# Optimization experiments

Hardware: AMD Instinct MI355X
Metric: run time of the kernel (lower is better)

Reference implementation:

```python
import jax, jax.numpy as jnp
import numpy as np

N, E = 50000, 300000
IN, FC, AC, H, C1, C2, OUT = 1024, 128, 20, 4, 10, 5, 3
FCN = FC + AC + H * C2  # 168


def bn_eval(x, g, b):
    # BatchNorm1d in eval mode with running_mean=0, running_var=1
    return x * (g / jnp.sqrt(1.0 + 1e-5)) + b


def add_self_loops(edge_index, edge_attr, n):
    # PyG add_self_loops with fill_value='mean': self-loop attr = mean of incoming edge attrs
    src, dst = edge_index[0], edge_index[1]
    ones = jnp.ones(src.shape[0], jnp.float32)
    deg = jax.ops.segment_sum(ones, dst, num_segments=n)
    mean_attr = jax.ops.segment_sum(edge_attr, dst, num_segments=n) / jnp.maximum(deg, 1.0)[:, None]
    loop = jnp.arange(n, dtype=src.dtype)
    return (jnp.concatenate([src, loop]), jnp.concatenate([dst, loop]),
            jnp.concatenate([edge_attr, mean_attr], 0))


def gatv2(x, src, dst, eattr, Wl, bl, Wr, br, We, att, b, n):
    # GATv2Conv (concat=True, negative_slope=0.2, edge_dim=1)
    h, c = att.shape
    xl = (x @ Wl + bl).reshape(n, h, c)
    xr = (x @ Wr + br).reshape(n, h, c)
    em = (eattr @ We).reshape(-1, h, c)
    m = jax.nn.leaky_relu(xl[src] + xr[dst] + em, 0.2)   # [E', H, C]
    logit = jnp.einsum('ehc,hc->eh', m, att)              # [E', H]
    mx = jax.ops.segment_max(logit, dst, num_segments=n)
    ex = jnp.exp(logit - mx[dst])
    den = jax.ops.segment_sum(ex, dst, num_segments=n)
    alpha = ex / (den[dst] + 1e-16)                       # segment softmax over dst
    out = jax.ops.segment_sum(xl[src] * alpha[..., None], dst, num_segments=n)
    return out.reshape(n, h * c) + b


def setup_inputs() -> dict:
    key = jax.random.key(0)
    ks = jax.random.split(key, 24)
    rn = lambda k, s: jax.random.normal(k, s, jnp.float32) * 0.05
    return {
        'features': jax.random.normal(ks[0], (N, IN), jnp.float32),
        'edges': jax.random.randint(ks[1], (2, E), 0, N),
        'edges2': jax.random.randint(ks[2], (2, E), 0, N),
        'edge_features': jax.random.normal(ks[3], (E, 1), jnp.float32),
        'additional_features': jax.random.normal(ks[4], (N, AC), jnp.float32),
        'sage_Wl': rn(ks[5], (IN, FC)), 'sage_bl': jnp.zeros((FC,), jnp.float32),
        'sage_Wr': rn(ks[6], (IN, FC)),
        'g1_Wl': rn(ks[7], (AC, H * C1)), 'g1_bl': jnp.zeros((H * C1,), jnp.float32),
        'g1_Wr': rn(ks[8], (AC, H * C1)), 'g1_br': jnp.zeros((H * C1,), jnp.float32),
        'g1_We': rn(ks[9], (1, H * C1)), 'g1_att': rn(ks[10], (H, C1)),
        'g1_b': jnp.zeros((H * C1,), jnp.float32),
        'g2_Wl': rn(ks[11], (H * C1, H * C2)), 'g2_bl': jnp.zeros((H * C2,), jnp.float32),
        'g2_Wr': rn(ks[12], (H * C1, H * C2)), 'g2_br': jnp.zeros((H * C2,), jnp.float32),
        'g2_We': rn(ks[13], (1, H * C2)), 'g2_att': rn(ks[14], (H, C2)),
        'g2_b': jnp.zeros((H * C2,), jnp.float32),
        'fc1_W': rn(ks[15], (FCN, FCN)), 'fc1_b': jnp.zeros((FCN,), jnp.float32),
        'fc2_W': rn(ks[16], (FCN, OUT)), 'fc2_b': jnp.zeros((OUT,), jnp.float32),
        'bnx_g': jnp.ones((FC,), jnp.float32), 'bnx_b': jnp.zeros((FC,), jnp.float32),
        'bny_g': jnp.ones((H * C2,), jnp.float32), 'bny_b': jnp.zeros((H * C2,), jnp.float32),
        'bnf_g': jnp.ones((FCN,), jnp.float32), 'bnf_b': jnp.zeros((FCN,), jnp.float32),
    }


def reference(features, edges, edges2, edge_features, additional_features,
              sage_Wl, sage_bl, sage_Wr,
              g1_Wl, g1_bl, g1_Wr, g1_br, g1_We, g1_att, g1_b,
              g2_Wl, g2_bl, g2_Wr, g2_br, g2_We, g2_att, g2_b,
              fc1_W, fc1_b, fc2_W, fc2_b,
              bnx_g, bnx_b, bny_g, bny_b, bnf_g, bnf_b):
    n = features.shape[0]
    # --- SAGEConv (mean aggr): out = lin_l(mean_j x_j) + lin_r(x_i) ---
    src, dst = edges[0], edges[1]
    deg = jax.ops.segment_sum(jnp.ones(src.shape[0], jnp.float32), dst, num_segments=n)
    aggr = jax.ops.segment_sum(features[src], dst, num_segments=n) / jnp.maximum(deg, 1.0)[:, None]
    x = aggr @ sage_Wl + sage_bl + features @ sage_Wr
    x = bn_eval(x, bnx_g, bnx_b)
    # --- GATv2 stack (self loops with mean edge-attr fill) ---
    s2, d2, ea = add_self_loops(edges2, edge_features, n)
    y = gatv2(additional_features, s2, d2, ea, g1_Wl, g1_bl, g1_Wr, g1_br, g1_We, g1_att, g1_b, n)
    y = jax.nn.leaky_relu(y, 0.01)  # activation (dropout off in eval)
    y = gatv2(y, s2, d2, ea, g2_Wl, g2_bl, g2_Wr, g2_br, g2_We, g2_att, g2_b, n)
    y = bn_eval(y, bny_g, bny_b)
    # --- MLP head ---
    z = jax.nn.leaky_relu(jnp.concatenate([x, y], axis=1), 0.01)
    z = jnp.concatenate([z, additional_features], axis=1) @ fc1_W + fc1_b
    z = jax.nn.relu(bn_eval(z, bnf_g, bnf_b))
    return z @ fc2_W + fc2_b
```

## Files before the change

### kernel.cpp

```cpp
#include <hip/hip_runtime.h>
#include <hip/hip_bf16.h>
#include <cfloat>

__device__ __forceinline__ float lrelu(float x, float a) { return x > 0.0f ? x : a * x; }

__device__ __forceinline__ unsigned short f2bf(float f) {
    unsigned u = __float_as_uint(f);
    unsigned r = (u + 0x7FFFu + ((u >> 16) & 1u)) >> 16;
    return (unsigned short)r;
}
__device__ __forceinline__ float bf2f(unsigned short u) {
    return __uint_as_float((unsigned)u << 16);
}

typedef __attribute__((ext_vector_type(8))) short short8;
typedef __attribute__((ext_vector_type(4))) float f32x4;

#define BN_RSQ 0.99999500003749968750f
#define SCAN_B 256

__global__ void zero_ws(uint4* __restrict__ p, int n16)
{
    int t = blockIdx.x * blockDim.x + threadIdx.x;
    if (t < n16) p[t] = make_uint4(0u, 0u, 0u, 0u);
}

__global__ void conv_wsage(const float* __restrict__ Wl, const float* __restrict__ Wr,
                           unsigned short* __restrict__ Btp)
{
    int idx = blockIdx.x * blockDim.x + threadIdx.x;
    if (idx >= 256 * 1024) return;
    int j    = idx & 7;
    int lane = (idx >> 3) & 63;
    int fn   = (idx >> 9) & 3;
    int wid  = (idx >> 11) & 3;
    int t    = idx >> 13;
    int c = wid * 64 + fn * 16 + (lane & 15);
    int k = t * 32 + (lane >> 4) * 8 + j;
    float v = (c < 128) ? Wl[(size_t)k * 128 + c] : Wr[(size_t)k * 128 + (c - 128)];
    Btp[idx] = f2bf(v);
}

__global__ void conv_wfc1(const float* __restrict__ fc1W, unsigned short* __restrict__ Bt1p)
{
    int idx = blockIdx.x * blockDim.x + threadIdx.x;
    if (idx >= 36864) return;
    int j    = idx & 7;
    int lane = (idx >> 3) & 63;
    int fn   = (idx >> 9) & 3;
    int q    = idx >> 11;
    int wid = q % 3, t = q / 3;
    int c = wid * 64 + fn * 16 + (lane & 15);
    int k = t * 32 + (lane >> 4) * 8 + j;
    float v = (c < 168 && k < 168) ? fc1W[(size_t)k * 168 + c] : 0.0f;
    Bt1p[idx] = f2bf(v);
}

__global__ __launch_bounds__(256) void gemm_sage_mfma(
    const float* __restrict__ A, const unsigned short* __restrict__ Btp,
    unsigned short* __restrict__ P, int M)
{
    __shared__ unsigned short As2[2][64][72];
    const int tid = threadIdx.x;
    const int wid = tid >> 6, lane = tid & 63;
    const int m0 = blockIdx.x * 64;
    const int l16 = lane & 15, g = lane >> 4;
    const int colbase = wid * 64 + l16;
    const short8* Bv = reinterpret_cast<const short8*>(Btp);
    const int srow = tid >> 4, scol = (tid & 15) * 4;

    f32x4 acc[4][4] = {};
    float4 rcur[4], rnext[4];

#pragma unroll
    for (int p = 0; p < 4; ++p) {
        int ar = m0 + p * 16 + srow;
        rcur[p] = make_float4(0.f, 0.f, 0.f, 0.f);
        if (ar < M) rcur[p] = *reinterpret_cast<const float4*>(&A[(size_t)ar * 1024 + scol]);
    }
#pragma unroll
    for (int p = 0; p < 4; ++p) {
        ushort4 u;
        u.x = f2bf(rcur[p].x); u.y = f2bf(rcur[p].y); u.z = f2bf(rcur[p].z); u.w = f2bf(rcur[p].w);
        *reinterpret_cast<ushort4*>(&As2[0][p * 16 + srow][scol]) = u;
    }
#pragma unroll
    for (int p = 0; p < 4; ++p) {
        int ar = m0 + p * 16 + srow;
        rcur[p] = make_float4(0.f, 0.f, 0.f, 0.f);
        if (ar < M) rcur[p] = *reinterpret_cast<const float4*>(&A[(size_t)ar * 1024 + 64 + scol]);
    }
    __syncthreads();

    for (int c = 0; c < 16; ++c) {
        const int buf = c & 1;
        short8 bfr[2][4];
#pragma unroll
        for (int t = 0; t < 2; ++t)
#pragma unroll
            for (int fn = 0; fn < 4; ++fn)
                bfr[t][fn] = Bv[(((c * 2 + t) * 4 + wid) * 4 + fn) * 64 + lane];
        __builtin_amdgcn_sched_barrier(0);
        if (c < 14) {
            const int k0 = (c + 2) * 64;
#pragma unroll
            for (int p = 0; p < 4; ++p) {
                int ar = m0 + p * 16 + srow;
                rnext[p] = make_float4(0.f, 0.f, 0.f, 0.f);
                if (ar < M) rnext[p] = *reinterpret_cast<const float4*>(&A[(size_t)ar * 1024 + k0 + scol]);
            }
        }
        __builtin_amdgcn_sched_barrier(0);
#pragma unroll
        for (int t = 0; t < 2; ++t) {
            short8 afr[4];
#pragma unroll
            for (int fm = 0; fm < 4; ++fm)
                afr[fm] = *reinterpret_cast<const short8*>(&As2[buf][fm * 16 + l16][t * 32 + g * 8]);
#pragma unroll
            for (int fm = 0; fm < 4; ++fm)
#pragma unroll
                for (int fn = 0; fn < 4; ++fn)
                    acc[fm][fn] = __builtin_amdgcn_mfma_f32_16x16x32_bf16(
                        afr[fm], bfr[t][fn], acc[fm][fn], 0, 0, 0);
        }
        if (c < 15) {
#pragma unroll
            for (int p = 0; p < 4; ++p) {
                ushort4 u;
                u.x = f2bf(rcur[p].x); u.y = f2bf(rcur[p].y);
                u.z = f2bf(rcur[p].z); u.w = f2bf(rcur[p].w);
                *reinterpret_cast<ushort4*>(&As2[buf ^ 1][p * 16 + srow][scol]) = u;
            }
        }
        __syncthreads();
#pragma unroll
        for (int p = 0; p < 4; ++p) rcur[p] = rnext[p];
    }

#pragma unroll
    for (int fm = 0; fm < 4; ++fm) {
#pragma unroll
        for (int r = 0; r < 4; ++r) {
            int row = m0 + fm * 16 + g * 4 + r;
            if (row < M) {
#pragma unroll
                for (int fn = 0; fn < 4; ++fn)
                    P[(size_t)row * 256 + colbase + fn * 16] = f2bf(acc[fm][fn][r]);
            }
        }
    }
}

__global__ __launch_bounds__(256) void mlp_mfma(
    const unsigned short* __restrict__ z, const float* __restrict__ addf,
    const unsigned short* __restrict__ Bt1p,
    const float* __restrict__ fc1b, const float* __restrict__ bnfg, const float* __restrict__ bnfb,
    const float* __restrict__ fc2W, const float* __restrict__ fc2b,
    float* __restrict__ out, int M)
{
    __shared__ __align__(16) char smem[64 * 169 * 4];
    unsigned short (*zs)[200] = reinterpret_cast<unsigned short(*)[200]>(smem);
    float (*ts)[169] = reinterpret_cast<float(*)[169]>(smem);
    const int tid = threadIdx.x;
    const int wid = tid >> 6, lane = tid & 63;
    const int m0 = blockIdx.x * 64;
    const int l16 = lane & 15, g = lane >> 4;
    const short8* Bv = reinterpret_cast<const short8*>(Bt1p);

#pragma unroll
    for (int p = 0; p < 13; ++p) {
        int idx = p * 256 + tid;
        if (idx < 3200) {
            int row = idx / 50, c4 = (idx % 50) * 4;
            int ar = m0 + row;
            ushort4 u; u.x = 0; u.y = 0; u.z = 0; u.w = 0;
            if (ar < M) {
                if (c4 < 148) {
                    u = *reinterpret_cast<const ushort4*>(&z[(size_t)ar * 168 + c4]);
                } else if (c4 < 168) {
                    float4 v = *reinterpret_cast<const float4*>(&addf[(size_t)ar * 20 + (c4 - 148)]);
                    u.x = f2bf(v.x); u.y = f2bf(v.y); u.z = f2bf(v.z); u.w = f2bf(v.w);
                }
            }
            *reinterpret_cast<ushort4*>(&zs[row][c4]) = u;
        }
    }
    __syncthreads();

    f32x4 acc[4][4] = {};
    if (wid < 3) {
#pragma unroll
        for (int t = 0; t < 6; ++t) {
            short8 afr[4], bfr[4];
#pragma unroll
            for (int fm = 0; fm < 4; ++fm)
                afr[fm] = *reinterpret_cast<const short8*>(&zs[fm * 16 + l16][t * 32 + g * 8]);
#pragma unroll
            for (int fn = 0; fn < 4; ++fn)
                bfr[fn] = Bv[((t * 3 + wid) * 4 + fn) * 64 + lane];
#pragma unroll
            for (int fm = 0; fm < 4; ++fm)
#pragma unroll
                for (int fn = 0; fn < 4; ++fn)
                    acc[fm][fn] = __builtin_amdgcn_mfma_f32_16x16x32_bf16(
                        afr[fm], bfr[fn], acc[fm][fn], 0, 0, 0);
        }
    }
    __syncthreads();
    if (wid < 3) {
        const int colbase = wid * 64 + l16;
#pragma unroll
        for (int fm = 0; fm < 4; ++fm) {
#pragma unroll
            for (int r = 0; r < 4; ++r) {
                int rr = fm * 16 + g * 4 + r;
#pragma unroll
                for (int fn = 0; fn < 4; ++fn) {
                    int col = colbase + fn * 16;
                    if (col < 168) {
                        float v = acc[fm][fn][r] + fc1b[col];
                        v = v * (bnfg[col] * BN_RSQ) + bnfb[col];
                        ts[rr][col] = fmaxf(v, 0.0f);
                    }
                }
            }
        }
    }
    __syncthreads();
    if (tid < 192) {
        int r = tid & 63, c = tid >> 6;
        float acc2 = fc2b[c];
#pragma unroll 4
        for (int k = 0; k < 168; ++k) acc2 += ts[r][k] * fc2W[k * 3 + c];
        int row = m0 + r;
        if (row < M) out[(size_t)row * 3 + c] = acc2;
    }
}

__global__ void edge_count(const int* __restrict__ e1d, const int* __restrict__ e2d,
                           const float* __restrict__ ef,
                           int* __restrict__ cnt1, int* __restrict__ cnt2,
                           float* __restrict__ easum, float* __restrict__ eaext, int E)
{
    int e = blockIdx.x * blockDim.x + threadIdx.x;
    if (e >= E) return;
    atomicAdd(&cnt1[e1d[e]], 1);
    int d2 = e2d[e];
    atomicAdd(&cnt2[d2], 1);
    float a = ef[e];
    atomicAdd(&easum[d2], a);
    eaext[e] = a;
}

__global__ void scan1(const int* __restrict__ cnt1, const int* __restrict__ cnt2,
                      int* __restrict__ off1, int* __restrict__ off2,
                      int* __restrict__ bsum1, int* __restrict__ bsum2, int M)
{
    __shared__ int sh[SCAN_B];
    int y = blockIdx.y;
    const int* cnt = y ? cnt2 : cnt1;
    int* excl = y ? off2 : off1;
    int* bsum = y ? bsum2 : bsum1;
    int i = blockIdx.x * SCAN_B + threadIdx.x;
    int v = (i < M) ? cnt[i] + y : 0;
    sh[threadIdx.x] = v;
    __syncthreads();
    for (int o = 1; o < SCAN_B; o <<= 1) {
        int t = (threadIdx.x >= o) ? sh[threadIdx.x - o] : 0;
        __syncthreads();
        sh[threadIdx.x] += t;
        __syncthreads();
    }
    if (i < M) excl[i] = sh[threadIdx.x] - v;
    if (threadIdx.x == SCAN_B - 1) bsum[blockIdx.x] = sh[threadIdx.x];
}

__global__ void scan2(int* __restrict__ bsum1, int* __restrict__ bsum2, int nb)
{
    __shared__ int sh[SCAN_B];
    int* bsum = blockIdx.y ? bsum2 : bsum1;
    int v = ((int)threadIdx.x < nb) ? bsum[threadIdx.x] : 0;
    sh[threadIdx.x] = v;
    __syncthreads();
    for (int o = 1; o < SCAN_B; o <<= 1) {
        int t = (threadIdx.x >= o) ? sh[threadIdx.x - o] : 0;
        __syncthreads();
        sh[threadIdx.x] += t;
        __syncthreads();
    }
    if ((int)threadIdx.x < nb) bsum[threadIdx.x] = sh[threadIdx.x] - v;
}

__global__ void scan3(int* __restrict__ off1, int* __restrict__ off2,
                      const int* __restrict__ bsum1, const int* __restrict__ bsum2,
                      const int* __restrict__ cnt1, const int* __restrict__ cnt2,
                      const float* __restrict__ easum, float* __restrict__ eaext,
                      int E, int M)
{
    int y = blockIdx.y;
    int* off = y ? off2 : off1;
    const int* bsum = y ? bsum2 : bsum1;
    const int* cnt = y ? cnt2 : cnt1;
    int i = blockIdx.x * SCAN_B + threadIdx.x;
    if (i < M) {
        int v = off[i] + bsum[blockIdx.x];
        off[i] = v;
        if (i == M - 1) off[M] = v + cnt[i] + y;
        if (y) eaext[E + i] = easum[i] / fmaxf((float)cnt2[i], 1.0f);
    }
}

__global__ void fill_both(const int* __restrict__ e1s, const int* __restrict__ e1d,
                          const int* __restrict__ e2d,
                          const int* __restrict__ off1, const int* __restrict__ off2,
                          int* __restrict__ cnt1, int* __restrict__ cnt2,
                          int* __restrict__ srcs1, int* __restrict__ eidx2, int E, int Eext)
{
    int t = blockIdx.x * blockDim.x + threadIdx.x;
    if (t < E) {
        int d = e1d[t];
        int pos = atomicSub(&cnt1[d], 1) - 1;
        srcs1[off1[d] + pos] = e1s[t];
    }
    int t2 = t - E;
    if (t2 >= 0 && t2 < Eext) {
        if (t2 < E) {
            int d = e2d[t2];
            int pos = atomicSub(&cnt2[d], 1) - 1;
            eidx2[off2[d] + pos] = t2;
        } else {
            int nn = t2 - E;
            eidx2[off2[nn + 1] - 1] = t2;
        }
    }
}

__global__ void sage_gather(const int* __restrict__ srcs1, const int* __restrict__ off1,
                            const unsigned short* __restrict__ P, const float* __restrict__ bl,
                            const float* __restrict__ bng, const float* __restrict__ bnb,
                            unsigned short* __restrict__ z, int N)
{
    int t = blockIdx.x * blockDim.x + threadIdx.x;
    if (t >= N * 32) return;
    int n = t >> 5, g = t & 31;
    int beg = off1[n], end = off1[n + 1];
    float a0 = 0.f, a1 = 0.f, a2 = 0.f, a3 = 0.f;
    for (int j = beg; j < end; ++j) {
        int s = srcs1[j];
        ushort4 v = *reinterpret_cast<const ushort4*>(&P[(size_t)s * 256 + g * 4]);
        a0 += bf2f(v.x); a1 += bf2f(v.y); a2 += bf2f(v.z); a3 += bf2f(v.w);
    }
    float inv = 1.0f / fmaxf((float)(end - beg), 1.0f);
    ushort4 pr = *reinterpret_cast<const ushort4*>(&P[(size_t)n * 256 + 128 + g * 4]);
    float a4[4] = {a0, a1, a2, a3};
    float p4[4] = {bf2f(pr.x), bf2f(pr.y), bf2f(pr.z), bf2f(pr.w)};
    ushort4 zo;
    unsigned short* zp = reinterpret_cast<unsigned short*>(&zo);
#pragma unroll
    for (int k = 0; k < 4; ++k) {
        int cc = g * 4 + k;
        float x = a4[k] * inv + bl[cc] + p4[k];
        x = x * (bng[cc] * BN_RSQ) + bnb[cc];
        zp[k] = f2bf(lrelu(x, 0.01f));
    }
    *reinterpret_cast<ushort4*>(&z[(size_t)n * 168 + g * 4]) = zo;
}

template <int IND, int HC>
__global__ void gat_lin(const float* __restrict__ X,
                        const float* __restrict__ Wl, const float* __restrict__ bl,
                        const float* __restrict__ Wr, const float* __restrict__ br,
                        float* __restrict__ xl, float* __restrict__ xr, int N)
{
    int t = blockIdx.x * blockDim.x + threadIdx.x;
    if (t >= N * HC) return;
    int n = t / HC, j = t % HC;
    float al = bl[j], ar = br[j];
    const float* xrow = X + (size_t)n * IND;
#pragma unroll 4
    for (int k = 0; k < IND; ++k) {
        float xv = xrow[k];
        al += xv * Wl[k * HC + j];
        ar += xv * Wr[k * HC + j];
    }
    xl[t] = al;
    xr[t] = ar;
}

template <int H, int C, int MODE>
__global__ void gat_node(const int* __restrict__ eidx2, const int* __restrict__ off2,
                         const int* __restrict__ e2s, const float* __restrict__ eaext,
                         const float* __restrict__ xl, const float* __restrict__ xr,
                         const float* __restrict__ We, const float* __restrict__ att,
                         const float* __restrict__ b,
                         const float* __restrict__ bng, const float* __restrict__ bnb,
                         void* __restrict__ outv, int E, int N)
{
    int t = blockIdx.x * blockDim.x + threadIdx.x;
    if (t >= N * H) return;
    int n = t / H, h = t % H;

    float xrc[C], atth[C], weh[C];
#pragma unroll
    for (int c = 0; c < C; ++c) {
        xrc[c]  = xr[(size_t)n * (H * C) + h * C + c];
        atth[c] = att[h * C + c];
        weh[c]  = We[h * C + c];
    }

    const int beg = off2[n], end = off2[n + 1];

    float mx = -FLT_MAX, den = 0.0f;
    float accv[C] = {};
    for (int j = beg; j < end; ++j) {
        int e = eidx2[j];
        int s = (e < E) ? e2s[e] : (e - E);
        float ea = eaext[e];
        const float* xls = xl + (size_t)s * (H * C) + h * C;
        float xv[C];
        float lg = 0.0f;
#pragma unroll
        for (int c = 0; c < C; ++c) {
            xv[c] = xls[c];
            float m = xv[c] + xrc[c] + ea * weh[c];
            lg += lrelu(m, 0.2f) * atth[c];
        }
        if (lg > mx) {
            float sc = __expf(mx - lg);
            den *= sc;
#pragma unroll
            for (int c = 0; c < C; ++c) accv[c] *= sc;
            mx = lg;
        }
        float ex = __expf(lg - mx);
        den += ex;
#pragma unroll
        for (int c = 0; c < C; ++c) accv[c] += ex * xv[c];
    }
    float inv = 1.0f / (den + 1e-16f);

#pragma unroll
    for (int c = 0; c < C; ++c) {
        int jch = h * C + c;
        float v = accv[c] * inv + b[jch];
        if (MODE == 1) {
            ((float*)outv)[(size_t)n * (H * C) + jch] = lrelu(v, 0.01f);
        } else {
            v = v * (bng[jch] * BN_RSQ) + bnb[jch];
            ((unsigned short*)outv)[(size_t)n * 168 + 128 + jch] = f2bf(lrelu(v, 0.01f));
        }
    }
}

extern "C" void kernel_launch(void* const* d_in, const int* in_sizes, int n_in,
                              void* d_out, int out_size, void* d_ws, size_t ws_size,
                              hipStream_t stream)
{
    const float* features = (const float*)d_in[0];
    const int*   e1       = (const int*)d_in[1];
    const int*   e2       = (const int*)d_in[2];
    const float* ef       = (const float*)d_in[3];
    const float* addf     = (const float*)d_in[4];
    const float* sage_Wl  = (const float*)d_in[5];
    const float* sage_bl  = (const float*)d_in[6];
    const float* sage_Wr  = (const float*)d_in[7];
    const float* g1_Wl = (const float*)d_in[8];
    const float* g1_bl = (const float*)d_in[9];
    const float* g1_Wr = (const float*)d_in[10];
    const float* g1_br = (const float*)d_in[11];
    const float* g1_We = (const float*)d_in[12];
    const float* g1_att = (const float*)d_in[13];
    const float* g1_b = (const float*)d_in[14];
    const float* g2_Wl = (const float*)d_in[15];
    const float* g2_bl = (const float*)d_in[16];
    const float* g2_Wr = (const float*)d_in[17];
    const float* g2_br = (const float*)d_in[18];
    const float* g2_We = (const float*)d_in[19];
    const float* g2_att = (const float*)d_in[20];
    const float* g2_b = (const float*)d_in[21];
    const float* fc1_W = (const float*)d_in[22];
    const float* fc1_b = (const float*)d_in[23];
    const float* fc2_W = (const float*)d_in[24];
    const float* fc2_b = (const float*)d_in[25];
    const float* bnx_g = (const float*)d_in[26];
    const float* bnx_b = (const float*)d_in[27];
    const float* bny_g = (const float*)d_in[28];
    const float* bny_b = (const float*)d_in[29];
    const float* bnf_g = (const float*)d_in[30];
    const float* bnf_b = (const float*)d_in[31];

    const int N = in_sizes[0] / 1024;
    const int E = in_sizes[3];
    const int Eext = E + N;
    const int* e1s = e1, *e1d = e1 + E;
    const int* e2s = e2, *e2d = e2 + E;
    const int nb = (N + SCAN_B - 1) / SCAN_B;

    char* wb = (char*)d_ws;
    size_t off = 0;
    auto takeB = [&](size_t bytes) { char* p = wb + off; off = (off + bytes + 255) & ~(size_t)255; return p; };
    unsigned short* P = (unsigned short*)takeB((size_t)N * 256 * 2);
    unsigned short* z = (unsigned short*)takeB((size_t)N * 168 * 2);
    float* eaext = (float*)takeB((size_t)Eext * 4);
    float* xl1   = (float*)takeB((size_t)N * 40 * 4);
    float* xr1   = (float*)takeB((size_t)N * 40 * 4);
    float* y1    = (float*)takeB((size_t)N * 40 * 4);
    float* xl2   = (float*)takeB((size_t)N * 20 * 4);
    float* xr2   = (float*)takeB((size_t)N * 20 * 4);
    unsigned short* Btp  = (unsigned short*)takeB((size_t)256 * 1024 * 2);
    unsigned short* Bt1p = (unsigned short*)takeB((size_t)36864 * 2);
    char* zero_beg = wb + off;
    int* cnt1    = (int*)takeB((size_t)N * 4);
    int* cnt2    = (int*)takeB((size_t)N * 4);
    float* easum = (float*)takeB((size_t)N * 4);
    size_t zero_len = (size_t)((wb + off) - zero_beg);
    int* off1  = (int*)takeB((size_t)(N + 1) * 4);
    int* off2  = (int*)takeB((size_t)(N + 1) * 4);
    int* bsum1 = (int*)takeB(SCAN_B * 4);
    int* bsum2 = (int*)takeB(SCAN_B * 4);
    int* srcs1 = (int*)takeB((size_t)E * 4);
    int* eidx2 = (int*)takeB((size_t)Eext * 4);

    const int B = 256;
    const int n16 = (int)(zero_len / 16);
    zero_ws<<<(n16 + B - 1) / B, B, 0, stream>>>((uint4*)zero_beg, n16);

    conv_wsage<<<(256 * 1024 + B - 1) / B, B, 0, stream>>>(sage_Wl, sage_Wr, Btp);
    conv_wfc1<<<(36864 + B - 1) / B, B, 0, stream>>>(fc1_W, Bt1p);

    edge_count<<<(E + B - 1) / B, B, 0, stream>>>(e1d, e2d, ef, cnt1, cnt2, easum, eaext, E);

    scan1<<<dim3(nb, 2), SCAN_B, 0, stream>>>(cnt1, cnt2, off1, off2, bsum1, bsum2, N);
    scan2<<<dim3(1, 2), SCAN_B, 0, stream>>>(bsum1, bsum2, nb);
    scan3<<<dim3(nb, 2), SCAN_B, 0, stream>>>(off1, off2, bsum1, bsum2, cnt1, cnt2,
                                              easum, eaext, E, N);

    fill_both<<<(E + Eext + B - 1) / B, B, 0, stream>>>(e1s, e1d, e2d, off1, off2,
                                                        cnt1, cnt2, srcs1, eidx2, E, Eext);

    const int mtiles = (N + 63) / 64;
    gemm_sage_mfma<<<mtiles, 256, 0, stream>>>(features, Btp, P, N);
    sage_gather<<<(N * 32 + B - 1) / B, B, 0, stream>>>(srcs1, off1, P, sage_bl, bnx_g, bnx_b, z, N);

    gat_lin<20, 40><<<(N * 40 + B - 1) / B, B, 0, stream>>>(addf, g1_Wl, g1_bl, g1_Wr, g1_br, xl1, xr1, N);
    gat_node<4, 10, 1><<<(N * 4 + B - 1) / B, B, 0, stream>>>(
        eidx2, off2, e2s, eaext, xl1, xr1, g1_We, g1_att, g1_b,
        nullptr, nullptr, (void*)y1, E, N);

    gat_lin<40, 20><<<(N * 20 + B - 1) / B, B, 0, stream>>>(y1, g2_Wl, g2_bl, g2_Wr, g2_br, xl2, xr2, N);
    gat_node<4, 5, 2><<<(N * 4 + B - 1) / B, B, 0, stream>>>(
        eidx2, off2, e2s, eaext, xl2, xr2, g2_We, g2_att, g2_b,
        bny_g, bny_b, (void*)z, E, N);

    mlp_mfma<<<mtiles, 256, 0, stream>>>(z, addf, Bt1p, fc1_b, bnf_g, bnf_b, fc2_W, fc2_b,
                                         (float*)d_out, N);
}
```

Baseline: 307.9 us.

## Retile SAGE GEMM into single-wave blocks with column-half split and grouped scheduling

Replaces the 4-wave 64x256 tile GEMM with single-wave 32x128 tiles, splitting the 256 output columns into two halves and interleaving row tiles in groups of eight so both halves read the same A rows close in time. Single-wave blocks remove __syncthreads and raise block count for better occupancy and latency hiding. The cost is that each A row is loaded and converted twice, relying on L2 for reuse, and prefetch depth drops to one stage.

```diff
diff --git a/kernel.cpp b/kernel.cpp
--- a/kernel.cpp
+++ b/kernel.cpp
@@ -56,97 +56,78 @@
     Bt1p[idx] = f2bf(v);
 }
 
-__global__ __launch_bounds__(256) void gemm_sage_mfma(
+__global__ __launch_bounds__(64) void gemm_sage_mfma(
     const float* __restrict__ A, const unsigned short* __restrict__ Btp,
-    unsigned short* __restrict__ P, int M)
-{
-    __shared__ unsigned short As2[2][64][72];
-    const int tid = threadIdx.x;
-    const int wid = tid >> 6, lane = tid & 63;
-    const int m0 = blockIdx.x * 64;
+    unsigned short* __restrict__ P, int M, int RT)
+{
+    __shared__ unsigned short As2[2][32][72];
+    const int lane = threadIdx.x;
+    const int idx  = blockIdx.x;
+    const int rowtile = (idx >> 4) * 8 + (idx & 7);
+    const int colhalf = (idx >> 3) & 1;
+    if (rowtile >= RT) return;
+    const int m0 = rowtile * 32;
     const int l16 = lane & 15, g = lane >> 4;
-    const int colbase = wid * 64 + l16;
     const short8* Bv = reinterpret_cast<const short8*>(Btp);
-    const int srow = tid >> 4, scol = (tid & 15) * 4;
-
-    f32x4 acc[4][4] = {};
-    float4 rcur[4], rnext[4];
-
-#pragma unroll
-    for (int p = 0; p < 4; ++p) {
-        int ar = m0 + p * 16 + srow;
-        rcur[p] = make_float4(0.f, 0.f, 0.f, 0.f);
-        if (ar < M) rcur[p] = *reinterpret_cast<const float4*>(&A[(size_t)ar * 1024 + scol]);
-    }
-#pragma unroll
-    for (int p = 0; p < 4; ++p) {
-        ushort4 u;
-        u.x = f2bf(rcur[p].x); u.y = f2bf(rcur[p].y); u.z = f2bf(rcur[p].z); u.w = f2bf(rcur[p].w);
-        *reinterpret_cast<ushort4*>(&As2[0][p * 16 + srow][scol]) = u;
-    }
-#pragma unroll
-    for (int p = 0; p < 4; ++p) {
-        int ar = m0 + p * 16 + srow;
-        rcur[p] = make_float4(0.f, 0.f, 0.f, 0.f);
-        if (ar < M) rcur[p] = *reinterpret_cast<const float4*>(&A[(size_t)ar * 1024 + 64 + scol]);
-    }
-    __syncthreads();
+
+    f32x4 acc[2][8] = {};
+    float4 rnext[8];
+
+    auto loadA = [&](int k0, float4 (&r)[8]) {
+#pragma unroll
+        for (int i = 0; i < 8; ++i) {
+            int ar = m0 + i * 4 + g;
+            r[i] = make_float4(0.f, 0.f, 0.f, 0.f);
+            if (ar < M) r[i] = *reinterpret_cast<const float4*>(&A[(size_t)ar * 1024 + k0 + l16 * 4]);
+        }
+    };
+    auto storeA = [&](int buf, const float4 (&r)[8]) {
+#pragma unroll
+        for (int i = 0; i < 8; ++i) {
+            int row = i * 4 + g;
+            ushort4 u;
+            u.x = f2bf(r[i].x); u.y = f2bf(r[i].y); u.z = f2bf(r[i].z); u.w = f2bf(r[i].w);
+            *reinterpret_cast<ushort4*>(&As2[buf][row][l16 * 4]) = u;
+        }
+    };
+
+    loadA(0, rnext);
+    storeA(0, rnext);
 
     for (int c = 0; c < 16; ++c) {
         const int buf = c & 1;
-        short8 bfr[2][4];
-#pragma unroll
-        for (int t = 0; t < 2; ++t)
-#pragma unroll
-            for (int fn = 0; fn < 4; ++fn)
-                bfr[t][fn] = Bv[(((c * 2 + t) * 4 + wid) * 4 + fn) * 64 + lane];
-        __builtin_amdgcn_sched_barrier(0);
-        if (c < 14) {
-            const int k0 = (c + 2) * 64;
-#pragma unroll
-            for (int p = 0; p < 4; ++p) {
-                int ar = m0 + p * 16 + srow;
-                rnext[p] = make_float4(0.f, 0.f, 0.f, 0.f);
-                if (ar < M) rnext[p] = *reinterpret_cast<const float4*>(&A[(size_t)ar * 1024 + k0 + scol]);
+        if (c < 15) loadA((c + 1) * 64, rnext);
+#pragma unroll
+        for (int t = 0; t < 2; ++t) {
+            const int ks = c * 2 + t;
+            short8 afr[2], bfr[8];
+#pragma unroll
+            for (int fm = 0; fm < 2; ++fm)
+                afr[fm] = *reinterpret_cast<const short8*>(&As2[buf][fm * 16 + l16][t * 32 + g * 8]);
+#pragma unroll
+            for (int fnn = 0; fnn < 8; ++fnn) {
+                int wo = colhalf * 2 + (fnn >> 2), fo = fnn & 3;
+                bfr[fnn] = Bv[((ks * 4 + wo) * 4 + fo) * 64 + lane];
             }
-        }
-        __builtin_amdgcn_sched_barrier(0);
-#pragma unroll
-        for (int t = 0; t < 2; ++t) {
-            short8 afr[4];
-#pragma unroll
-            for (int fm = 0; fm < 4; ++fm)
-                afr[fm] = *reinterpret_cast<const short8*>(&As2[buf][fm * 16 + l16][t * 32 + g * 8]);
-#pragma unroll
-            for (int fm = 0; fm < 4; ++fm)
-#pragma unroll
-                for (int fn = 0; fn < 4; ++fn)
-                    acc[fm][fn] = __builtin_amdgcn_mfma_f32_16x16x32_bf16(
-                        afr[fm], bfr[t][fn], acc[fm][fn], 0, 0, 0);
-        }
-        if (c < 15) {
-#pragma unroll
-            for (int p = 0; p < 4; ++p) {
-                ushort4 u;
-                u.x = f2bf(rcur[p].x); u.y = f2bf(rcur[p].y);
-                u.z = f2bf(rcur[p].z); u.w = f2bf(rcur[p].w);
-                *reinterpret_cast<ushort4*>(&As2[buf ^ 1][p * 16 + srow][scol]) = u;
-            }
-        }
-        __syncthreads();
-#pragma unroll
-        for (int p = 0; p < 4; ++p) rcur[p] = rnext[p];
-    }
-
-#pragma unroll
-    for (int fm = 0; fm < 4; ++fm) {
-#pragma unroll
-        for (int r = 0; r < 4; ++r) {
-            int row = m0 + fm * 16 + g * 4 + r;
+#pragma unroll
+            for (int fm = 0; fm < 2; ++fm)
+#pragma unroll
+                for (int fnn = 0; fnn < 8; ++fnn)
+                    acc[fm][fnn] = __builtin_amdgcn_mfma_f32_16x16x32_bf16(
+                        afr[fm], bfr[fnn], acc[fm][fnn], 0, 0, 0);
+        }
+        if (c < 15) storeA(buf ^ 1, rnext);
+    }
+
+#pragma unroll
+    for (int fm = 0; fm < 2; ++fm) {
+#pragma unroll
+        for (int rr = 0; rr < 4; ++rr) {
+            int row = m0 + fm * 16 + g * 4 + rr;
             if (row < M) {
 #pragma unroll
-                for (int fn = 0; fn < 4; ++fn)
-                    P[(size_t)row * 256 + colbase + fn * 16] = f2bf(acc[fm][fn][r]);
+                for (int fnn = 0; fnn < 8; ++fnn)
+                    P[(size_t)row * 256 + colhalf * 128 + fnn * 16 + l16] = f2bf(acc[fm][fnn][rr]);
             }
         }
     }
@@ -539,8 +520,9 @@
     fill_both<<<(E + Eext + B - 1) / B, B, 0, stream>>>(e1s, e1d, e2d, off1, off2,
                                                         cnt1, cnt2, srcs1, eidx2, E, Eext);
 
-    const int mtiles = (N + 63) / 64;
-    gemm_sage_mfma<<<mtiles, 256, 0, stream>>>(features, Btp, P, N);
+    const int RT = (N + 31) / 32;
+    const int RTp = (RT + 7) & ~7;
+    gemm_sage_mfma<<<RTp * 2, 64, 0, stream>>>(features, Btp, P, N, RT);
     sage_gather<<<(N * 32 + B - 1) / B, B, 0, stream>>>(srcs1, off1, P, sage_bl, bnx_g, bnx_b, z, N);
 
     gat_lin<20, 40><<<(N * 40 + B - 1) / B, B, 0, stream>>>(addf, g1_Wl, g1_bl, g1_Wr, g1_br, xl1, xr1, N);
@@ -553,6 +535,7 @@
         eidx2, off2, e2s, eaext, xl2, xr2, g2_We, g2_att, g2_b,
         bny_g, bny_b, (void*)z, E, N);
 
+    const int mtiles = (N + 63) / 64;
     mlp_mfma<<<mtiles, 256, 0, stream>>>(z, addf, Bt1p, fc1_b, bnf_g, bnf_b, fc2_W, fc2_b,
                                          (float*)d_out, N);
 }
```

Result: slower. 335.7 us, median of 2 (+9.0%).
